# Kernel optimization log

Measured on AMD Instinct MI355X. Metric: run time of the kernel, lower is better.

Reference implementation:

```python
import jax, jax.numpy as jnp
import numpy as np

ALPHA = 1.0          # temperature of the Bayesian DP (init kwarg alpha)
NEG = -1e9           # -inf surrogate, safe in fp32/bf16


def conv1d_same(x, w, b):
    # x: [B, T, Cin], w: [K, Cin, Cout], 'SAME' padding, stride 1
    y = jax.lax.conv_general_dilated(x, w, window_strides=(1,), padding='SAME',
                                     dimension_numbers=('NWC', 'WIO', 'NWC'))
    return y + b


def postnet(x, ws, bs):
    # Tacotron-style conv PostNet: n_conv conv1d layers with tanh (dropout=0, eval mode)
    for w, b in zip(ws, bs):
        x = jnp.tanh(conv1d_same(x, w, b))
    return x


def bayesian_dp(W, alpha):
    """Monotonic-alignment Bayesian DP (Gumbel propagation).

    W: [B, T, S] node weights on the alignment grid (T = mel time, S = text).
    Each node (t, s) has two parents: (t-1, s) [stay] and (t-1, s-1) [advance].
      mu[t,s] = W[t,s] + (1/alpha) * logsumexp(alpha*mu[t-1,s], alpha*mu[t-1,s-1])
      pi[t,s] = softmax over the two parents -> [B, T, S, 2]
    """
    B, T, S = W.shape
    m0 = W[:, 0] + jnp.where(jnp.arange(S) == 0, 0.0, NEG)   # path must start at (0,0)
    pi0 = jnp.broadcast_to(jnp.array([1.0, 0.0], W.dtype), (B, S, 2))

    def step(prev, w_t):
        # prev: [B, S] = mu[t-1]; shifted: mu[t-1, s-1]
        shifted = jnp.concatenate([jnp.full((B, 1), NEG, prev.dtype), prev[:, :-1]], axis=1)
        stacked = jnp.stack([prev, shifted], axis=-1)         # [B, S, 2]
        m = w_t + jax.nn.logsumexp(alpha * stacked, axis=-1) / alpha
        pi_t = jax.nn.softmax(alpha * stacked, axis=-1)
        return m, (m, pi_t)

    _, (ms, pis) = jax.lax.scan(step, m0, jnp.swapaxes(W, 0, 1)[1:])  # scan over T-1
    mu = jnp.concatenate([m0[:, None], jnp.swapaxes(ms, 0, 1)], axis=1)    # [B, T, S]
    pi = jnp.concatenate([pi0[:, None], jnp.swapaxes(pis, 0, 1)], axis=1)  # [B, T, S, 2]
    return mu, pi


def setup_inputs() -> dict:
    key = jax.random.key(0)
    ks = jax.random.split(key, 6)
    B, T, S = 32, 2000, 400
    NMELS, H, K = 80, 256, 5
    inputs = jax.random.normal(ks[0], (B, T, NMELS), dtype=jnp.float32)
    src_enc = jax.random.normal(ks[1], (B, S, H), dtype=jnp.float32)
    mask = jnp.ones((B, T, S), dtype=jnp.float32)
    w1 = jax.random.normal(ks[2], (K, NMELS, H), dtype=jnp.float32) * 0.05
    w2 = jax.random.normal(ks[3], (K, H, H), dtype=jnp.float32) * 0.05
    w3 = jax.random.normal(ks[4], (K, H, H), dtype=jnp.float32) * 0.05
    b1 = jnp.zeros((H,), jnp.float32)
    b2 = jnp.zeros((H,), jnp.float32)
    b3 = jnp.zeros((H,), jnp.float32)
    return {"inputs": inputs, "src_enc": src_enc, "mask": mask,
            "w1": w1, "b1": b1, "w2": w2, "b2": b2, "w3": w3, "b3": b3}


def reference(inputs, src_enc, mask, w1, b1, w2, b2, w3, b3):
    # PostNet over mel frames -> spec embeddings matching src_enc dim
    Wspec = postnet(inputs, [w1, w2, w3], [b1, b2, b3])       # [B, T, H]
    # attention score grid
    W = jnp.einsum('bth,bsh->bts', Wspec, src_enc)            # [B, T, S]
    alignments = jax.nn.softmax(W, axis=1)                    # softmax over mel-time (dim 1)
    mu, pi = bayesian_dp(alignments * mask, ALPHA)
    return mu, pi, alignments, Wspec
```

## Files before the change

kernel.cpp:

```cpp
#include <hip/hip_runtime.h>
#include <hip/hip_bf16.h>

#define B_ 32
#define T_ 2000
#define S_ 400
#define C0_ 80
#define H_ 256

static constexpr float NEGV = -1e9f;
static constexpr int NMU  = B_ * T_ * S_;
static constexpr int NPI  = 2 * NMU;

typedef _Float16 f16x8 __attribute__((ext_vector_type(8)));
typedef float    f32x4 __attribute__((ext_vector_type(4)));

__global__ __launch_bounds__(256)
void wprep(const float* __restrict__ w, _Float16* __restrict__ wcat,
           int CIN, int CPAD)
{
  const int tot = 256 * 5 * CPAD;
  int idx = blockIdx.x * 256 + threadIdx.x;
  if (idx >= tot) return;
  int co  = idx / (5 * CPAD);
  int rem = idx - co * (5 * CPAD);
  int k   = rem / CPAD;
  int ci  = rem - k * CPAD;
  float v = (ci < CIN) ? w[((size_t)k * CIN + ci) * H_ + co] : 0.f;
  wcat[idx] = (_Float16)v;
}

__global__ __launch_bounds__(256)
void ecast(const float* __restrict__ e, _Float16* __restrict__ ef)
{
  const int n4 = B_ * S_ * H_ / 4;
  int idx = blockIdx.x * 256 + threadIdx.x;
  if (idx >= n4) return;
  float4 v = ((const float4*)e)[idx];
  _Float16* d = ef + (size_t)idx * 4;
  d[0] = (_Float16)v.x; d[1] = (_Float16)v.y;
  d[2] = (_Float16)v.z; d[3] = (_Float16)v.w;
}

template<int CIN, int CPAD, bool INF32, bool OUTF32>
__global__ __launch_bounds__(256)
void conv_mfma(const void* __restrict__ xin, const _Float16* __restrict__ wcat,
               const float* __restrict__ bias, void* __restrict__ yout)
{
  constexpr int KK  = 5 * CPAD;
  constexpr int NS  = KK / 32;
  constexpr int STR = CPAD + 8;
  __shared__ _Float16 xs[68 * STR];
  const int b   = blockIdx.y;
  const int t0  = blockIdx.x * 64;
  const int tid = threadIdx.x;
  const int w   = tid >> 6;
  const int l   = tid & 63;

  if constexpr (INF32) {
    const float* xb = (const float*)xin + (size_t)b * T_ * CIN;
    constexpr int NG = CPAD / 4;
    for (int idx = tid; idx < 68 * NG; idx += 256) {
      int j = idx / NG, g = idx - j * NG;
      int t = t0 - 2 + j;
      int c = g * 4;
      float4 v = make_float4(0.f, 0.f, 0.f, 0.f);
      if (t >= 0 && t < T_ && c < CIN) v = *(const float4*)&xb[(size_t)t * CIN + c];
      _Float16* d = &xs[j * STR + c];
      d[0] = (_Float16)v.x; d[1] = (_Float16)v.y;
      d[2] = (_Float16)v.z; d[3] = (_Float16)v.w;
    }
  } else {
    const _Float16* xb = (const _Float16*)xin + (size_t)b * T_ * CIN;
    constexpr int NG = CPAD / 8;
    for (int idx = tid; idx < 68 * NG; idx += 256) {
      int j = idx / NG, g = idx - j * NG;
      int t = t0 - 2 + j;
      f16x8 v = {(_Float16)0,(_Float16)0,(_Float16)0,(_Float16)0,
                 (_Float16)0,(_Float16)0,(_Float16)0,(_Float16)0};
      if (t >= 0 && t < T_) v = *(const f16x8*)&xb[(size_t)t * CIN + g * 8];
      *(f16x8*)&xs[j * STR + g * 8] = v;
    }
  }
  __syncthreads();

  const int lr = l & 15;
  const int lk = (l >> 4) * 8;

  f32x4 acc[4][4];
  const f32x4 zz = {0.f, 0.f, 0.f, 0.f};
#pragma unroll
  for (int i = 0; i < 4; i++)
#pragma unroll
    for (int j = 0; j < 4; j++) acc[i][j] = zz;

  const _Float16* wbase = wcat + (size_t)(w * 64 + lr) * KK + lk;

  for (int kk = 0; kk < NS; kk++) {
    const int p  = kk * 32;
    const int k  = p / CPAD;
    const int ci = p - k * CPAD;
    f16x8 a0 = *(const f16x8*)&xs[( 0 + lr + k) * STR + ci + lk];
    f16x8 a1 = *(const f16x8*)&xs[(16 + lr + k) * STR + ci + lk];
    f16x8 a2 = *(const f16x8*)&xs[(32 + lr + k) * STR + ci + lk];
    f16x8 a3 = *(const f16x8*)&xs[(48 + lr + k) * STR + ci + lk];
    f16x8 w0 = *(const f16x8*)&wbase[(size_t)( 0) * KK + p];
    f16x8 w1 = *(const f16x8*)&wbase[(size_t)(16) * KK + p];
    f16x8 w2 = *(const f16x8*)&wbase[(size_t)(32) * KK + p];
    f16x8 w3 = *(const f16x8*)&wbase[(size_t)(48) * KK + p];
    acc[0][0] = __builtin_amdgcn_mfma_f32_16x16x32_f16(a0, w0, acc[0][0], 0, 0, 0);
    acc[0][1] = __builtin_amdgcn_mfma_f32_16x16x32_f16(a0, w1, acc[0][1], 0, 0, 0);
    acc[0][2] = __builtin_amdgcn_mfma_f32_16x16x32_f16(a0, w2, acc[0][2], 0, 0, 0);
    acc[0][3] = __builtin_amdgcn_mfma_f32_16x16x32_f16(a0, w3, acc[0][3], 0, 0, 0);
    acc[1][0] = __builtin_amdgcn_mfma_f32_16x16x32_f16(a1, w0, acc[1][0], 0, 0, 0);
    acc[1][1] = __builtin_amdgcn_mfma_f32_16x16x32_f16(a1, w1, acc[1][1], 0, 0, 0);
    acc[1][2] = __builtin_amdgcn_mfma_f32_16x16x32_f16(a1, w2, acc[1][2], 0, 0, 0);
    acc[1][3] = __builtin_amdgcn_mfma_f32_16x16x32_f16(a1, w3, acc[1][3], 0, 0, 0);
    acc[2][0] = __builtin_amdgcn_mfma_f32_16x16x32_f16(a2, w0, acc[2][0], 0, 0, 0);
    acc[2][1] = __builtin_amdgcn_mfma_f32_16x16x32_f16(a2, w1, acc[2][1], 0, 0, 0);
    acc[2][2] = __builtin_amdgcn_mfma_f32_16x16x32_f16(a2, w2, acc[2][2], 0, 0, 0);
    acc[2][3] = __builtin_amdgcn_mfma_f32_16x16x32_f16(a2, w3, acc[2][3], 0, 0, 0);
    acc[3][0] = __builtin_amdgcn_mfma_f32_16x16x32_f16(a3, w0, acc[3][0], 0, 0, 0);
    acc[3][1] = __builtin_amdgcn_mfma_f32_16x16x32_f16(a3, w1, acc[3][1], 0, 0, 0);
    acc[3][2] = __builtin_amdgcn_mfma_f32_16x16x32_f16(a3, w2, acc[3][2], 0, 0, 0);
    acc[3][3] = __builtin_amdgcn_mfma_f32_16x16x32_f16(a3, w3, acc[3][3], 0, 0, 0);
  }

#pragma unroll
  for (int ct = 0; ct < 4; ct++) {
    const int co = w * 64 + ct * 16 + lr;
    const float bv = bias[co];
#pragma unroll
    for (int tt = 0; tt < 4; tt++) {
#pragma unroll
      for (int r = 0; r < 4; r++) {
        const int t = t0 + tt * 16 + (l >> 4) * 4 + r;
        if (t < T_) {
          float v = tanhf(acc[tt][ct][r] + bv);
          if constexpr (OUTF32)
            ((float*)yout)[((size_t)b * T_ + t) * H_ + co] = v;
          else
            ((_Float16*)yout)[((size_t)b * T_ + t) * H_ + co] = (_Float16)v;
        }
      }
    }
  }
}

__global__ __launch_bounds__(256)
void einsum_mfma(const float* __restrict__ A, const _Float16* __restrict__ E,
                 float* __restrict__ Wg,
                 float* __restrict__ pm, float* __restrict__ pl)
{
  constexpr int STR = H_ + 8;
  __shared__ _Float16 xs[64 * STR];
  const int b   = blockIdx.z;
  const int t0  = blockIdx.x * 64;
  const int s0  = blockIdx.y * 256;
  const int tid = threadIdx.x;
  const int w   = tid >> 6;
  const int l   = tid & 63;

  const float* Ab = A + (size_t)b * T_ * H_;
  for (int idx = tid; idx < 64 * 64; idx += 256) {
    int row = idx >> 6, g = idx & 63;
    int t = t0 + row;
    float4 v = make_float4(0.f, 0.f, 0.f, 0.f);
    if (t < T_) v = *(const float4*)&Ab[(size_t)t * H_ + 4 * g];
    _Float16* d = &xs[row * STR + 4 * g];
    d[0] = (_Float16)v.x; d[1] = (_Float16)v.y;
    d[2] = (_Float16)v.z; d[3] = (_Float16)v.w;
  }
  __syncthreads();

  const int lr = l & 15;
  const int lk = (l >> 4) * 8;

  f32x4 acc[4][4];
  const f32x4 zz = {0.f, 0.f, 0.f, 0.f};
#pragma unroll
  for (int i = 0; i < 4; i++)
#pragma unroll
    for (int j = 0; j < 4; j++) acc[i][j] = zz;

  const _Float16* Eb = E + (size_t)b * S_ * H_;
  const int sr = s0 + w * 64 + lr;
  const _Float16* e0 = Eb + (size_t)((sr      < S_) ? sr      : (S_ - 1)) * H_ + lk;
  const _Float16* e1 = Eb + (size_t)((sr + 16 < S_) ? sr + 16 : (S_ - 1)) * H_ + lk;
  const _Float16* e2 = Eb + (size_t)((sr + 32 < S_) ? sr + 32 : (S_ - 1)) * H_ + lk;
  const _Float16* e3 = Eb + (size_t)((sr + 48 < S_) ? sr + 48 : (S_ - 1)) * H_ + lk;

#pragma unroll
  for (int kk = 0; kk < 8; kk++) {
    const int p = kk * 32;
    f16x8 a0 = *(const f16x8*)&xs[( 0 + lr) * STR + p + lk];
    f16x8 a1 = *(const f16x8*)&xs[(16 + lr) * STR + p + lk];
    f16x8 a2 = *(const f16x8*)&xs[(32 + lr) * STR + p + lk];
    f16x8 a3 = *(const f16x8*)&xs[(48 + lr) * STR + p + lk];
    f16x8 w0 = *(const f16x8*)&e0[p];
    f16x8 w1 = *(const f16x8*)&e1[p];
    f16x8 w2 = *(const f16x8*)&e2[p];
    f16x8 w3 = *(const f16x8*)&e3[p];
    acc[0][0] = __builtin_amdgcn_mfma_f32_16x16x32_f16(a0, w0, acc[0][0], 0, 0, 0);
    acc[0][1] = __builtin_amdgcn_mfma_f32_16x16x32_f16(a0, w1, acc[0][1], 0, 0, 0);
    acc[0][2] = __builtin_amdgcn_mfma_f32_16x16x32_f16(a0, w2, acc[0][2], 0, 0, 0);
    acc[0][3] = __builtin_amdgcn_mfma_f32_16x16x32_f16(a0, w3, acc[0][3], 0, 0, 0);
    acc[1][0] = __builtin_amdgcn_mfma_f32_16x16x32_f16(a1, w0, acc[1][0], 0, 0, 0);
    acc[1][1] = __builtin_amdgcn_mfma_f32_16x16x32_f16(a1, w1, acc[1][1], 0, 0, 0);
    acc[1][2] = __builtin_amdgcn_mfma_f32_16x16x32_f16(a1, w2, acc[1][2], 0, 0, 0);
    acc[1][3] = __builtin_amdgcn_mfma_f32_16x16x32_f16(a1, w3, acc[1][3], 0, 0, 0);
    acc[2][0] = __builtin_amdgcn_mfma_f32_16x16x32_f16(a2, w0, acc[2][0], 0, 0, 0);
    acc[2][1] = __builtin_amdgcn_mfma_f32_16x16x32_f16(a2, w1, acc[2][1], 0, 0, 0);
    acc[2][2] = __builtin_amdgcn_mfma_f32_16x16x32_f16(a2, w2, acc[2][2], 0, 0, 0);
    acc[2][3] = __builtin_amdgcn_mfma_f32_16x16x32_f16(a2, w3, acc[2][3], 0, 0, 0);
    acc[3][0] = __builtin_amdgcn_mfma_f32_16x16x32_f16(a3, w0, acc[3][0], 0, 0, 0);
    acc[3][1] = __builtin_amdgcn_mfma_f32_16x16x32_f16(a3, w1, acc[3][1], 0, 0, 0);
    acc[3][2] = __builtin_amdgcn_mfma_f32_16x16x32_f16(a3, w2, acc[3][2], 0, 0, 0);
    acc[3][3] = __builtin_amdgcn_mfma_f32_16x16x32_f16(a3, w3, acc[3][3], 0, 0, 0);
  }

  float* Wb = Wg + (size_t)b * T_ * S_;
#pragma unroll
  for (int ct = 0; ct < 4; ct++) {
    const int s = s0 + w * 64 + ct * 16 + lr;
    if (s < S_) {
#pragma unroll
      for (int tt = 0; tt < 4; tt++) {
#pragma unroll
        for (int r = 0; r < 4; r++) {
          const int t = t0 + tt * 16 + (l >> 4) * 4 + r;
          if (t < T_) Wb[(size_t)t * S_ + s] = acc[tt][ct][r];
        }
      }
    }
  }

  const int tblk = blockIdx.x;
#pragma unroll
  for (int ct = 0; ct < 4; ct++) {
    float M = -3e38f;
#pragma unroll
    for (int tt = 0; tt < 4; tt++)
#pragma unroll
      for (int r = 0; r < 4; r++) {
        const int t = t0 + tt * 16 + (l >> 4) * 4 + r;
        if (t < T_) M = fmaxf(M, acc[tt][ct][r]);
      }
    float L = 0.f;
#pragma unroll
    for (int tt = 0; tt < 4; tt++)
#pragma unroll
      for (int r = 0; r < 4; r++) {
        const int t = t0 + tt * 16 + (l >> 4) * 4 + r;
        if (t < T_) L += __expf(acc[tt][ct][r] - M);
      }
#pragma unroll
    for (int mk = 16; mk <= 32; mk <<= 1) {
      float Mo = __shfl_xor(M, mk);
      float Lo = __shfl_xor(L, mk);
      float Mn = fmaxf(M, Mo);
      L = L * __expf(M - Mn) + Lo * __expf(Mo - Mn);
      M = Mn;
    }
    if ((l >> 4) == 0) {
      const int s = s0 + w * 64 + ct * 16 + lr;
      if (s < S_) {
        pm[((size_t)b * 32 + tblk) * S_ + s] = M;
        pl[((size_t)b * 32 + tblk) * S_ + s] = L;
      }
    }
  }
}

__global__ __launch_bounds__(256)
void stats_reduce(const float* __restrict__ pm, const float* __restrict__ pl,
                  float* __restrict__ statsOut)
{
  int idx = blockIdx.x * 256 + threadIdx.x;
  if (idx >= B_ * S_) return;
  int b = idx / S_, s = idx - b * S_;
  float M = -3e38f, L = 0.f;
#pragma unroll 4
  for (int k = 0; k < 32; k++) {
    float m = pm[((size_t)b * 32 + k) * S_ + s];
    float l = pl[((size_t)b * 32 + k) * S_ + s];
    float Mn = fmaxf(M, m);
    L = L * __expf(M - Mn) + l * __expf(m - Mn);
    M = Mn;
  }
  statsOut[(size_t)b * S_ + s] = M + __logf(L);
}

__global__ __launch_bounds__(256)
void norm_kernel(float* __restrict__ al, const float* __restrict__ Mk,
                 const float* __restrict__ stats, float* __restrict__ wdp)
{
  constexpr float C2 = 1.44269504f;
  const int gid = blockIdx.x * 256 + threadIdx.x;
  if (gid >= NMU / 4) return;
  const int b   = gid / (T_ * S_ / 4);
  const int rem = gid - b * (T_ * S_ / 4);
  const int s4  = rem % (S_ / 4);
  const float4 st4 = *(const float4*)&stats[(size_t)b * S_ + 4 * s4];
  float4 r = ((const float4*)al)[gid];
  float4 k = ((const float4*)Mk)[gid];
  float4 a;
  a.x = __expf(r.x - st4.x);
  a.y = __expf(r.y - st4.y);
  a.z = __expf(r.z - st4.z);
  a.w = __expf(r.w - st4.w);
  ((float4*)al)[gid] = a;
  ((float4*)wdp)[gid] = make_float4(a.x * k.x * C2, a.y * k.y * C2,
                                    a.z * k.z * C2, a.w * k.w * C2);
}

__global__ __launch_bounds__(256, 1)
void dp_skew2(const float* Wdp, float* muOut, float* piOut)
{
  __shared__ float ring[64 * S_];
  __shared__ float bnd[32][4];
  const int b = blockIdx.x;
  const int w = threadIdx.x >> 6;
  const int l = threadIdx.x & 63;
  const int lc = (l < 50) ? l : 49;
  const bool act = (l < 50);
  const int sc = 100 * w + 2 * lc;

  const float* wb  = Wdp   + (size_t)b * T_ * S_;
  float*       mub = muOut + (size_t)b * T_ * S_;
  float*       pib = piOut + (size_t)(2 * b) * T_ * S_;

  constexpr float LN2  = 0.693147181f;
  constexpr float NEGN = -1.44269504e9f;

#define DMA(row)                                                            \
  { const char* s_ = (const char*)(wb + (size_t)(row) * S_);                \
    char* d_ = (char*)ring + (((row) & 63) * 1600);                         \
    __builtin_amdgcn_global_load_lds(                                       \
      (const __attribute__((address_space(1))) void*)(s_ + l * 16),         \
      (__attribute__((address_space(3))) void*)(d_ + l * 16), 16, 0, 0);    \
    if (l < 36)                                                             \
      __builtin_amdgcn_global_load_lds(                                     \
        (const __attribute__((address_space(1))) void*)(s_ + 1024 + l*16),  \
        (__attribute__((address_space(3))) void*)(d_ + 1024 + l*16), 16, 0, 0); }

#pragma unroll
  for (int i = 0; i < 6; ++i) { const int r0 = 6 * w + i; DMA(r0) }
  asm volatile("s_waitcnt vmcnt(0)" ::: "memory");
  __syncthreads();

  float n0 = NEGN, n1 = NEGN;

  for (int p = 0; p <= 253; ++p) {
    __builtin_amdgcn_s_barrier();
    const int j = p - w - 1;

    {
      const int dr = 8 * p + 24 + 2 * w;
      if (dr < T_) DMA(dr)
      const int dr1 = dr + 1;
      if (dr1 < T_) DMA(dr1)
    }

    if (p == w) {
      float2 c0v = *(const float2*)&ring[sc];
      n0 = c0v.x + ((sc == 0) ? 0.f : NEGN);
      n1 = c0v.y + NEGN;
      if (act) {
        *(float2*)&mub[sc] = make_float2(n0 * LN2, n1 * LN2);
        *(float4*)&pib[2 * sc] = make_float4(1.f, 0.f, 1.f, 0.f);
      }
      if (l == 49) bnd[0][w] = n1;
    } else if (j >= 0 && j <= 249) {
      const int tb = 8 * j + 1;
      float2 cur[8];
      float  bq[8];
#pragma unroll
      for (int k = 0; k < 8; ++k) {
        const int t = tb + k;
        cur[k] = (t < T_) ? *(const float2*)&ring[(t & 63) * S_ + sc]
                          : make_float2(0.f, 0.f);
        bq[k] = (w > 0) ? bnd[(t - 1) & 31][w - 1] : NEGN;
      }
      float* mrow = mub + (size_t)tb * S_ + sc;
      float* prow = pib + (size_t)tb * (2 * S_) + 2 * sc;
#pragma unroll
      for (int k = 0; k < 8; ++k) {
        const int t = tb + k;
        if (t < T_) {
          float sh = __shfl_up(n1, 1);
          float sft0 = (l == 0) ? bq[k] : sh;
          float d0 = n0 - sft0;
          float e0; asm("v_exp_f32 %0, %1" : "=v"(e0) : "v"(-fabsf(d0)));
          float q0 = 1.f + e0;
          float lg0; asm("v_log_f32 %0, %1" : "=v"(lg0) : "v"(q0));
          float rc0; asm("v_rcp_f32 %0, %1" : "=v"(rc0) : "v"(q0));
          float p00 = (d0 >= 0.f) ? rc0 : 1.f - rc0;
          float nn0 = cur[k].x + fmaxf(n0, sft0) + lg0;
          float d1 = n1 - n0;
          float e1; asm("v_exp_f32 %0, %1" : "=v"(e1) : "v"(-fabsf(d1)));
          float q1 = 1.f + e1;
          float lg1; asm("v_log_f32 %0, %1" : "=v"(lg1) : "v"(q1));
          float rc1; asm("v_rcp_f32 %0, %1" : "=v"(rc1) : "v"(q1));
          float p01 = (d1 >= 0.f) ? rc1 : 1.f - rc1;
          float nn1 = cur[k].y + fmaxf(n1, n0) + lg1;
          if (act) {
            *(float2*)mrow = make_float2(nn0 * LN2, nn1 * LN2);
            *(float4*)prow = make_float4(p00, 1.f - p00, p01, 1.f - p01);
          }
          n0 = nn0; n1 = nn1;
          if (l == 49) bnd[t & 31][w] = n1;
        }
        mrow += S_;
        prow += 2 * S_;
      }
    }
    asm volatile("s_waitcnt lgkmcnt(0)" ::: "memory");
    asm volatile("s_waitcnt vmcnt(56)" ::: "memory");
  }
#undef DMA
}

extern "C" void kernel_launch(void* const* d_in, const int* in_sizes, int n_in,
                              void* d_out, int out_size, void* d_ws, size_t ws_size,
                              hipStream_t stream)
{
  (void)in_sizes; (void)n_in; (void)out_size; (void)d_ws; (void)ws_size;
  const float* x   = (const float*)d_in[0];
  const float* enc = (const float*)d_in[1];
  const float* msk = (const float*)d_in[2];
  const float* w1  = (const float*)d_in[3];
  const float* b1  = (const float*)d_in[4];
  const float* w2  = (const float*)d_in[5];
  const float* b2  = (const float*)d_in[6];
  const float* w3  = (const float*)d_in[7];
  const float* b3  = (const float*)d_in[8];

  float* out = (float*)d_out;
  float* mu  = out;
  float* pi  = out + NMU;
  float* al  = out + NMU + NPI;
  float* wsp = out + NMU + NPI + NMU;

  _Float16*  h1  = (_Float16*)(pi + 26000000);
  _Float16*  h2  = (_Float16*)(pi + 35000000);
  _Float16*  wc1 = (_Float16*)(pi + 44000000);
  _Float16*  wc2 = (_Float16*)(pi + 44100000);
  _Float16*  wc3 = (_Float16*)(pi + 44300000);
  _Float16*  encf = (_Float16*)(pi + 44600000);
  float*     pm   = pi + 46300000;
  float*     pl   = pi + 47200000;
  float*     pistats = pi + NPI - 13056;

  hipLaunchKernelGGL(wprep, dim3((256*5*96 +255)/256), dim3(256), 0, stream, w1, wc1, C0_, 96);
  hipLaunchKernelGGL(wprep, dim3((256*5*256+255)/256), dim3(256), 0, stream, w2, wc2, H_, 256);
  hipLaunchKernelGGL(wprep, dim3((256*5*256+255)/256), dim3(256), 0, stream, w3, wc3, H_, 256);
  hipLaunchKernelGGL(ecast, dim3(B_*S_*H_/4/256), dim3(256), 0, stream, enc, encf);

  dim3 cgrid((T_ + 63) / 64, B_);
  hipLaunchKernelGGL((conv_mfma<C0_,  96, true,  false>), cgrid, dim3(256), 0, stream,
                     (const void*)x,  wc1, b1, (void*)h1);
  hipLaunchKernelGGL((conv_mfma<H_,  256, false, false>), cgrid, dim3(256), 0, stream,
                     (const void*)h1, wc2, b2, (void*)h2);
  hipLaunchKernelGGL((conv_mfma<H_,  256, false, true >), cgrid, dim3(256), 0, stream,
                     (const void*)h2, wc3, b3, (void*)wsp);

  hipLaunchKernelGGL(einsum_mfma, dim3((T_ + 63) / 64, (S_ + 255) / 256, B_), dim3(256),
                     0, stream, wsp, encf, al, pm, pl);
  hipLaunchKernelGGL(stats_reduce, dim3((B_ * S_ + 255) / 256), dim3(256), 0, stream,
                     pm, pl, pistats);
  hipLaunchKernelGGL(norm_kernel, dim3(NMU / 4 / 256), dim3(256), 0, stream, al, msk, pistats, mu);
  hipLaunchKernelGGL(dp_skew2, dim3(B_), dim3(256), 0, stream, mu, mu, pi);
}
```

Measured before the change: 1.039 ms.

## Pack two batch DP wavefront groups per workgroup with smaller LDS ring

The DP kernel now runs two independent batch elements per 512-thread workgroup, each with its own 48-row LDS ring and boundary buffer, launching B/2 blocks instead of B. The prefetch distance is cut and slot indexing becomes an explicit modular counter, with vmcnt waits adjusted to match. The aim is to interleave two latency-bound serial recurrences on one CU so transcendental and memory latency is hidden better. The cost is that only 16 CUs are used and a shallower prefetch may expose global load latency.

Measured after the change: 1.119 ms. +7.7%, slower.

```diff
diff --git a/kernel.cpp b/kernel.cpp
--- a/kernel.cpp
+++ b/kernel.cpp
@@ -313,17 +313,18 @@
                                     a.z * k.z * C2, a.w * k.w * C2);
 }
 
-__global__ __launch_bounds__(256, 1)
-void dp_skew2(const float* Wdp, float* muOut, float* piOut)
-{
-  __shared__ float ring[64 * S_];
-  __shared__ float bnd[32][4];
-  const int b = blockIdx.x;
-  const int w = threadIdx.x >> 6;
-  const int l = threadIdx.x & 63;
-  const int lc = (l < 50) ? l : 49;
+__global__ __launch_bounds__(512, 1)
+void dp_dual(const float* Wdp, float* muOut, float* piOut)
+{
+  __shared__ float ring[2][48 * S_];
+  __shared__ float bnd[2][32][4];
+  const int grp = threadIdx.x >> 8;
+  const int w   = (threadIdx.x >> 6) & 3;
+  const int l   = threadIdx.x & 63;
+  const int b   = blockIdx.x * 2 + grp;
+  const int lc  = (l < 50) ? l : 49;
   const bool act = (l < 50);
-  const int sc = 100 * w + 2 * lc;
+  const int sc  = 100 * w + 2 * lc;
 
   const float* wb  = Wdp   + (size_t)b * T_ * S_;
   float*       mub = muOut + (size_t)b * T_ * S_;
@@ -332,9 +333,9 @@
   constexpr float LN2  = 0.693147181f;
   constexpr float NEGN = -1.44269504e9f;
 
-#define DMA(row)                                                            \
+#define DMA(row, slot)                                                      \
   { const char* s_ = (const char*)(wb + (size_t)(row) * S_);                \
-    char* d_ = (char*)ring + (((row) & 63) * 1600);                         \
+    char* d_ = (char*)&ring[grp][0] + ((slot) * 1600);                      \
     __builtin_amdgcn_global_load_lds(                                       \
       (const __attribute__((address_space(1))) void*)(s_ + l * 16),         \
       (__attribute__((address_space(3))) void*)(d_ + l * 16), 16, 0, 0);    \
@@ -343,33 +344,35 @@
         (const __attribute__((address_space(1))) void*)(s_ + 1024 + l*16),  \
         (__attribute__((address_space(3))) void*)(d_ + 1024 + l*16), 16, 0, 0); }
 
-#pragma unroll
-  for (int i = 0; i < 6; ++i) { const int r0 = 6 * w + i; DMA(r0) }
+  DMA(2 * w,     2 * w)
+  DMA(2 * w + 1, 2 * w + 1)
   asm volatile("s_waitcnt vmcnt(0)" ::: "memory");
   __syncthreads();
 
   float n0 = NEGN, n1 = NEGN;
+  int ds = 8 + 2 * w;
+  int rs = 1;
 
   for (int p = 0; p <= 253; ++p) {
     __builtin_amdgcn_s_barrier();
     const int j = p - w - 1;
 
     {
-      const int dr = 8 * p + 24 + 2 * w;
-      if (dr < T_) DMA(dr)
-      const int dr1 = dr + 1;
-      if (dr1 < T_) DMA(dr1)
+      const int dr = 8 * p + 8 + 2 * w;
+      if (dr < T_)     DMA(dr, ds)
+      if (dr + 1 < T_) DMA(dr + 1, ds + 1)
+      ds += 8; if (ds >= 48) ds -= 48;
     }
 
     if (p == w) {
-      float2 c0v = *(const float2*)&ring[sc];
+      float2 c0v = *(const float2*)&ring[grp][sc];
       n0 = c0v.x + ((sc == 0) ? 0.f : NEGN);
       n1 = c0v.y + NEGN;
       if (act) {
         *(float2*)&mub[sc] = make_float2(n0 * LN2, n1 * LN2);
         *(float4*)&pib[2 * sc] = make_float4(1.f, 0.f, 1.f, 0.f);
       }
-      if (l == 49) bnd[0][w] = n1;
+      if (l == 49) bnd[grp][0][w] = n1;
     } else if (j >= 0 && j <= 249) {
       const int tb = 8 * j + 1;
       float2 cur[8];
@@ -377,9 +380,10 @@
 #pragma unroll
       for (int k = 0; k < 8; ++k) {
         const int t = tb + k;
-        cur[k] = (t < T_) ? *(const float2*)&ring[(t & 63) * S_ + sc]
+        int sk = rs + k; if (sk >= 48) sk -= 48;
+        cur[k] = (t < T_) ? *(const float2*)&ring[grp][sk * S_ + sc]
                           : make_float2(0.f, 0.f);
-        bq[k] = (w > 0) ? bnd[(t - 1) & 31][w - 1] : NEGN;
+        bq[k] = (w > 0) ? bnd[grp][(t - 1) & 31][w - 1] : NEGN;
       }
       float* mrow = mub + (size_t)tb * S_ + sc;
       float* prow = pib + (size_t)tb * (2 * S_) + 2 * sc;
@@ -408,14 +412,16 @@
             *(float4*)prow = make_float4(p00, 1.f - p00, p01, 1.f - p01);
           }
           n0 = nn0; n1 = nn1;
-          if (l == 49) bnd[t & 31][w] = n1;
+          if (l == 49) bnd[grp][t & 31][w] = n1;
         }
         mrow += S_;
         prow += 2 * S_;
       }
+      rs += 8; if (rs >= 48) rs -= 48;
     }
     asm volatile("s_waitcnt lgkmcnt(0)" ::: "memory");
-    asm volatile("s_waitcnt vmcnt(56)" ::: "memory");
+    if (p < 4) { asm volatile("s_waitcnt vmcnt(0)"  ::: "memory"); }
+    else       { asm volatile("s_waitcnt vmcnt(16)" ::: "memory"); }
   }
 #undef DMA
 }
@@ -469,5 +475,5 @@
   hipLaunchKernelGGL(stats_reduce, dim3((B_ * S_ + 255) / 256), dim3(256), 0, stream,
                      pm, pl, pistats);
   hipLaunchKernelGGL(norm_kernel, dim3(NMU / 4 / 256), dim3(256), 0, stream, al, msk, pistats, mu);
-  hipLaunchKernelGGL(dp_skew2, dim3(B_), dim3(256), 0, stream, mu, mu, pi);
-}
+  hipLaunchKernelGGL(dp_dual, dim3(B_ / 2), dim3(512), 0, stream, mu, mu, pi);
+}
```

## Deepen DP wavefront stages to 16 rows with 96-slot LDS ring

Applied to the files above, without the earlier changes.

The skewed DP kernel now handles 16 time rows per stage instead of 8. This halves the number of barrier-separated stages, so fewer barriers are paid across the 2000-row recurrence. The LDS ring grows to 96 rows and the boundary buffer to 64 entries, with explicit slot indices replacing the power-of-two masks. The vmcnt wait is moved to the top of each iteration. In exchange, the skew pipeline takes longer to fill and drain, register use rises from the 16-element arrays, and there is more LDS pressure.

After: 926.1 us, median of 2. -10.9%, faster.

```diff
diff --git a/kernel.cpp b/kernel.cpp
--- a/kernel.cpp
+++ b/kernel.cpp
@@ -314,10 +314,10 @@
 }
 
 __global__ __launch_bounds__(256, 1)
-void dp_skew2(const float* Wdp, float* muOut, float* piOut)
-{
-  __shared__ float ring[64 * S_];
-  __shared__ float bnd[32][4];
+void dp_skew3(const float* Wdp, float* muOut, float* piOut)
+{
+  __shared__ float ring[96 * S_];
+  __shared__ float bnd[64][4];
   const int b = blockIdx.x;
   const int w = threadIdx.x >> 6;
   const int l = threadIdx.x & 63;
@@ -332,9 +332,9 @@
   constexpr float LN2  = 0.693147181f;
   constexpr float NEGN = -1.44269504e9f;
 
-#define DMA(row)                                                            \
+#define DMA(row, slot)                                                      \
   { const char* s_ = (const char*)(wb + (size_t)(row) * S_);                \
-    char* d_ = (char*)ring + (((row) & 63) * 1600);                         \
+    char* d_ = (char*)ring + ((slot) * 1600);                               \
     __builtin_amdgcn_global_load_lds(                                       \
       (const __attribute__((address_space(1))) void*)(s_ + l * 16),         \
       (__attribute__((address_space(3))) void*)(d_ + l * 16), 16, 0, 0);    \
@@ -344,21 +344,30 @@
         (__attribute__((address_space(3))) void*)(d_ + 1024 + l*16), 16, 0, 0); }
 
 #pragma unroll
-  for (int i = 0; i < 6; ++i) { const int r0 = 6 * w + i; DMA(r0) }
+  for (int i = 0; i < 4; ++i) { const int r0 = 4 * w + i; DMA(r0, r0) }
+  if (w == 0) DMA(16, 16)
   asm volatile("s_waitcnt vmcnt(0)" ::: "memory");
   __syncthreads();
 
   float n0 = NEGN, n1 = NEGN;
-
-  for (int p = 0; p <= 253; ++p) {
+  int rs = 1;
+  int ds = 17 + 4 * w;
+
+  for (int p = 0; p <= 128; ++p) {
     __builtin_amdgcn_s_barrier();
+    asm volatile("s_waitcnt vmcnt(40)" ::: "memory");
     const int j = p - w - 1;
 
     {
-      const int dr = 8 * p + 24 + 2 * w;
-      if (dr < T_) DMA(dr)
-      const int dr1 = dr + 1;
-      if (dr1 < T_) DMA(dr1)
+      const int dr = 16 * (p + 1) + 1 + 4 * w;
+#pragma unroll
+      for (int q = 0; q < 4; ++q) {
+        if (dr + q < T_) {
+          int s2 = ds + q; if (s2 >= 96) s2 -= 96;
+          DMA(dr + q, s2)
+        }
+      }
+      ds += 16; if (ds >= 96) ds -= 96;
     }
 
     if (p == w) {
@@ -370,21 +379,22 @@
         *(float4*)&pib[2 * sc] = make_float4(1.f, 0.f, 1.f, 0.f);
       }
       if (l == 49) bnd[0][w] = n1;
-    } else if (j >= 0 && j <= 249) {
-      const int tb = 8 * j + 1;
-      float2 cur[8];
-      float  bq[8];
-#pragma unroll
-      for (int k = 0; k < 8; ++k) {
+    } else if (j >= 0 && j <= 124) {
+      const int tb = 16 * j + 1;
+      float2 cur[16];
+      float  bq[16];
+#pragma unroll
+      for (int k = 0; k < 16; ++k) {
         const int t = tb + k;
-        cur[k] = (t < T_) ? *(const float2*)&ring[(t & 63) * S_ + sc]
+        int sk = rs + k; if (sk >= 96) sk -= 96;
+        cur[k] = (t < T_) ? *(const float2*)&ring[sk * S_ + sc]
                           : make_float2(0.f, 0.f);
-        bq[k] = (w > 0) ? bnd[(t - 1) & 31][w - 1] : NEGN;
+        bq[k] = (w > 0) ? bnd[(t - 1) & 63][w - 1] : NEGN;
       }
       float* mrow = mub + (size_t)tb * S_ + sc;
       float* prow = pib + (size_t)tb * (2 * S_) + 2 * sc;
 #pragma unroll
-      for (int k = 0; k < 8; ++k) {
+      for (int k = 0; k < 16; ++k) {
         const int t = tb + k;
         if (t < T_) {
           float sh = __shfl_up(n1, 1);
@@ -408,14 +418,14 @@
             *(float4*)prow = make_float4(p00, 1.f - p00, p01, 1.f - p01);
           }
           n0 = nn0; n1 = nn1;
-          if (l == 49) bnd[t & 31][w] = n1;
+          if (l == 49) bnd[t & 63][w] = n1;
         }
         mrow += S_;
         prow += 2 * S_;
       }
+      rs += 16; if (rs >= 96) rs -= 96;
     }
     asm volatile("s_waitcnt lgkmcnt(0)" ::: "memory");
-    asm volatile("s_waitcnt vmcnt(56)" ::: "memory");
   }
 #undef DMA
 }
@@ -469,5 +479,5 @@
   hipLaunchKernelGGL(stats_reduce, dim3((B_ * S_ + 255) / 256), dim3(256), 0, stream,
                      pm, pl, pistats);
   hipLaunchKernelGGL(norm_kernel, dim3(NMU / 4 / 256), dim3(256), 0, stream, al, msk, pistats, mu);
-  hipLaunchKernelGGL(dp_skew2, dim3(B_), dim3(256), 0, stream, mu, mu, pi);
-}
+  hipLaunchKernelGGL(dp_skew3, dim3(B_), dim3(256), 0, stream, mu, mu, pi);
+}
```
